# Kernel tuning notes

Measured on AMD Instinct MI355X. Metric: run time of the kernel, lower is better.

## Reference

```python
import jax, jax.numpy as jnp
import numpy as np

N_NODES = 20000
N_EDGES = 640000
D_IN = 128
D_HID = 128


def setup_inputs() -> dict:
    key = jax.random.key(0)
    ks = jax.random.split(key, 10)
    s_in = 1.0 / np.sqrt(D_IN).astype(np.float32)
    s_hid = 1.0 / np.sqrt(D_HID).astype(np.float32)
    return {
        "h": jax.random.normal(ks[0], (N_NODES, D_IN), jnp.float32),
        "edge_index": jax.random.randint(ks[1], (2, N_EDGES), 0, N_NODES, jnp.int32),
        "W0": jax.random.normal(ks[2], (D_IN, D_HID), jnp.float32) * s_in,
        "b0": jnp.zeros((D_HID,), jnp.float32),
        "W1": jax.random.normal(ks[3], (D_HID, D_HID), jnp.float32) * s_hid,
        "b1": jnp.zeros((D_HID,), jnp.float32),
        "W2": jax.random.normal(ks[4], (D_HID, D_HID), jnp.float32) * s_hid,
        "b2": jnp.zeros((D_HID,), jnp.float32),
        "W3": jax.random.normal(ks[5], (D_HID, D_HID), jnp.float32) * s_hid,
        "b3": jnp.zeros((D_HID,), jnp.float32),
    }


def reference(h, edge_index, W0, b0, W1, b1, W2, b2, W3, b3):
    # GIN forward: num_layers-1 = 4 GINConv layers, each
    # h' = Linear((1+eps)*h + sum_{j->i} h_j) with eps = 0.
    src = edge_index[0]
    dst = edge_index[1]
    n = h.shape[0]
    for W, b in ((W0, b0), (W1, b1), (W2, b2), (W3, b3)):
        # sparse sum-aggregation over edges: gather source features, scatter-add to dst
        agg = jax.ops.segment_sum(h[src], dst, num_segments=n)  # [N, D]
        h = (h + agg) @ W + b  # dense per-node MLP (single Linear)
    return h
```

## Files before the change

kernel.cpp:

```cpp
#include <hip/hip_runtime.h>

#define N_NODES 20000
#define N_EDGES 640000
#define D 128
#define CAP 128
#define NB_AGG 40000
#define NB_CHAIN 129
#define SPMV_BLOCKS 313
#define NB_SCAT 625
#define NB_H2BF 1250
#define TM 32

typedef unsigned int uint;
typedef unsigned short ushort;

__device__ __forceinline__ float bflo(uint u) { return __uint_as_float(u << 16); }
__device__ __forceinline__ float bfhi(uint u) { return __uint_as_float(u & 0xffff0000u); }
__device__ __forceinline__ uint pack2bf(float lo, float hi) {
    uint a = __float_as_uint(lo), b = __float_as_uint(hi);
    a += 0x7fffu + ((a >> 16) & 1u);
    b += 0x7fffu + ((b >> 16) & 1u);
    return (a >> 16) | (b & 0xffff0000u);
}


__global__ void zero_cnt_kernel(int* __restrict__ cnt) {
    int i = blockIdx.x * blockDim.x + threadIdx.x;
    if (i < N_NODES) cnt[i] = 0;
}


__global__ void scatter_h2bf_kernel(const int4* __restrict__ src4, const int4* __restrict__ dst4,
                                    int* __restrict__ cnt, ushort* __restrict__ slot,
                                    const float4* __restrict__ hin, uint4* __restrict__ hbf) {
    int bid = blockIdx.x;
    int t = threadIdx.x;
    if (bid < NB_SCAT) {
        int e4 = bid * 256 + t;
        int4 s = src4[e4];
        int4 d = dst4[e4];
        slot[d.x * CAP + atomicAdd(&cnt[d.x], 1)] = (ushort)s.x;
        slot[d.y * CAP + atomicAdd(&cnt[d.y], 1)] = (ushort)s.y;
        slot[d.z * CAP + atomicAdd(&cnt[d.z], 1)] = (ushort)s.z;
        slot[d.w * CAP + atomicAdd(&cnt[d.w], 1)] = (ushort)s.w;
    } else {
        int i = (bid - NB_SCAT) * 256 + t;
        float4 f0 = hin[i * 2];
        float4 f1 = hin[i * 2 + 1];
        uint4 o;
        o.x = pack2bf(f0.x, f0.y); o.y = pack2bf(f0.z, f0.w);
        o.z = pack2bf(f1.x, f1.y); o.w = pack2bf(f1.z, f1.w);
        hbf[i] = o;
    }
}


__global__ __launch_bounds__(64) void agg_fused_kernel(
        const uint4* __restrict__ hbf, const int* __restrict__ cnt,
        const ushort* __restrict__ slot, uint4* __restrict__ xbf,
        const float* __restrict__ cA, const float* __restrict__ cbias,
        const float* __restrict__ cB, float* __restrict__ cO,
        const float* __restrict__ uin, float* __restrict__ uout) {
    int bid = blockIdx.x;
    int t = threadIdx.x;

    if (bid >= NB_AGG) {
        int cb = bid - NB_AGG;
        if (cO && cb < NB_CHAIN) {
            const float* Ar = (cb < 128) ? &cA[cb * 128] : cbias;
            int c0 = t, c1 = t + 64;
            float s0 = 0.f, s1 = 0.f;
            for (int k = 0; k < 128; ++k) {
                float a = Ar[k];
                s0 += a * cB[k * 128 + c0];
                s1 += a * cB[k * 128 + c1];
            }
            cO[cb * 128 + c0] = s0;
            cO[cb * 128 + c1] = s1;
        } else if (uout) {
            int sb = cb - (cO ? NB_CHAIN : 0);
            int node = sb * 64 + t;
            if (node < N_NODES) {
                int c = cnt[node];
                const ushort* sl = &slot[node * CAP];
                float s;
                if (uin) {
                    s = uin[node];
                    for (int k = 0; k < c; ++k) s += uin[sl[k]];
                } else {
                    s = 1.0f + 2.0f * (float)c;
                    for (int k = 0; k < c; ++k) s += (float)cnt[sl[k]];
                }
                uout[node] = s;
            }
        }
        return;
    }

    int r = bid & 7;
    int q = bid >> 3;
    int slice = r >> 2;
    int node  = q * 4 + (r & 3);
    int lo = node * CAP;
    int hi = lo + cnt[node];
    int slot8 = t >> 3;
    int fl    = t & 7;
    int soff  = slice * 8 + fl;

    uint4 sv = hbf[(size_t)node * 16 + soff];

    float a0 = 0.f, a1 = 0.f, a2 = 0.f, a3 = 0.f;
    float a4 = 0.f, a5 = 0.f, a6 = 0.f, a7 = 0.f;

#define ACC8(v) do { \
        a0 += bflo((v).x); a1 += bfhi((v).x); \
        a2 += bflo((v).y); a3 += bfhi((v).y); \
        a4 += bflo((v).z); a5 += bfhi((v).z); \
        a6 += bflo((v).w); a7 += bfhi((v).w); } while (0)

    int k = lo + slot8;
    for (; k + 24 < hi; k += 32) {
        int s0 = slot[k];
        int s1 = slot[k + 8];
        int s2 = slot[k + 16];
        int s3 = slot[k + 24];
        uint4 v0 = hbf[(size_t)s0 * 16 + soff];
        uint4 v1 = hbf[(size_t)s1 * 16 + soff];
        uint4 v2 = hbf[(size_t)s2 * 16 + soff];
        uint4 v3 = hbf[(size_t)s3 * 16 + soff];
        ACC8(v0); ACC8(v1); ACC8(v2); ACC8(v3);
    }
    for (; k < hi; k += 8) {
        int s0 = slot[k];
        uint4 v0 = hbf[(size_t)s0 * 16 + soff];
        ACC8(v0);
    }
#undef ACC8

    a0 += __shfl_xor(a0, 8);  a1 += __shfl_xor(a1, 8);
    a2 += __shfl_xor(a2, 8);  a3 += __shfl_xor(a3, 8);
    a4 += __shfl_xor(a4, 8);  a5 += __shfl_xor(a5, 8);
    a6 += __shfl_xor(a6, 8);  a7 += __shfl_xor(a7, 8);
    a0 += __shfl_xor(a0, 16); a1 += __shfl_xor(a1, 16);
    a2 += __shfl_xor(a2, 16); a3 += __shfl_xor(a3, 16);
    a4 += __shfl_xor(a4, 16); a5 += __shfl_xor(a5, 16);
    a6 += __shfl_xor(a6, 16); a7 += __shfl_xor(a7, 16);
    a0 += __shfl_xor(a0, 32); a1 += __shfl_xor(a1, 32);
    a2 += __shfl_xor(a2, 32); a3 += __shfl_xor(a3, 32);
    a4 += __shfl_xor(a4, 32); a5 += __shfl_xor(a5, 32);
    a6 += __shfl_xor(a6, 32); a7 += __shfl_xor(a7, 32);

    if (t < 8) {
        a0 += bflo(sv.x); a1 += bfhi(sv.x);
        a2 += bflo(sv.y); a3 += bfhi(sv.y);
        a4 += bflo(sv.z); a5 += bfhi(sv.z);
        a6 += bflo(sv.w); a7 += bfhi(sv.w);
        uint4 o;
        o.x = pack2bf(a0, a1); o.y = pack2bf(a2, a3);
        o.z = pack2bf(a4, a5); o.w = pack2bf(a6, a7);
        xbf[(size_t)node * 16 + soff] = o;
    }
}


__global__ __launch_bounds__(256) void gemm_kernel(const uint4* __restrict__ xb,
                                                   const float* __restrict__ W,
                                                   float* __restrict__ out,
                                                   const int* __restrict__ cnt,
                                                   const float* __restrict__ ub,
                                                   const float* __restrict__ uc,
                                                   const float* __restrict__ v2p,
                                                   const float* __restrict__ v3p,
                                                   const float* __restrict__ v4p,
                                                   const float* __restrict__ v1p) {
    __shared__ float Xs[TM][D];
    int t = threadIdx.x;
    int row0 = blockIdx.x * TM;

    for (int i = t; i < TM * 16; i += 256) {
        int rr  = i >> 4;
        int c16 = i & 15;
        uint4 u = xb[(size_t)(row0 + rr) * 16 + c16];
        float4 f0 = make_float4(bflo(u.x), bfhi(u.x), bflo(u.y), bfhi(u.y));
        float4 f1 = make_float4(bflo(u.z), bfhi(u.z), bflo(u.w), bfhi(u.w));
        *((float4*)&Xs[rr][c16 * 8])     = f0;
        *((float4*)&Xs[rr][c16 * 8 + 4]) = f1;
    }
    __syncthreads();

    int cg = t & 31;
    int rg = t >> 5;
    int j0 = cg * 4;
    int r0 = rg * 4;

    float acc[4][4];
    #pragma unroll
    for (int i = 0; i < 4; ++i) {
        acc[i][0] = 0.f; acc[i][1] = 0.f; acc[i][2] = 0.f; acc[i][3] = 0.f;
    }

    for (int k4 = 0; k4 < D; k4 += 4) {
        float4 w0 = *((const float4*)&W[(k4 + 0) * D + j0]);
        float4 w1 = *((const float4*)&W[(k4 + 1) * D + j0]);
        float4 w2 = *((const float4*)&W[(k4 + 2) * D + j0]);
        float4 w3 = *((const float4*)&W[(k4 + 3) * D + j0]);
        #pragma unroll
        for (int i = 0; i < 4; ++i) {
            float4 xv = *((const float4*)&Xs[r0 + i][k4]);
            acc[i][0] += xv.x * w0.x; acc[i][0] += xv.y * w1.x;
            acc[i][0] += xv.z * w2.x; acc[i][0] += xv.w * w3.x;
            acc[i][1] += xv.x * w0.y; acc[i][1] += xv.y * w1.y;
            acc[i][1] += xv.z * w2.y; acc[i][1] += xv.w * w3.y;
            acc[i][2] += xv.x * w0.z; acc[i][2] += xv.y * w1.z;
            acc[i][2] += xv.z * w2.z; acc[i][2] += xv.w * w3.z;
            acc[i][3] += xv.x * w0.w; acc[i][3] += xv.y * w1.w;
            acc[i][3] += xv.z * w2.w; acc[i][3] += xv.w * w3.w;
        }
    }

    float4 v1 = *((const float4*)&v1p[j0]);
    float4 v2 = *((const float4*)&v2p[j0]);
    float4 v3 = *((const float4*)&v3p[j0]);
    float4 v4 = *((const float4*)&v4p[j0]);

    #pragma unroll
    for (int i = 0; i < 4; ++i) {
        int ra = row0 + r0 + i;
        float aa = 1.0f + (float)cnt[ra];
        float ab = ub[ra], ac = uc[ra];
        float o0 = acc[i][0] + ac * v4.x + ab * v3.x + aa * v2.x + v1.x;
        float o1 = acc[i][1] + ac * v4.y + ab * v3.y + aa * v2.y + v1.y;
        float o2 = acc[i][2] + ac * v4.z + ab * v3.z + aa * v2.z + v1.z;
        float o3 = acc[i][3] + ac * v4.w + ab * v3.w + aa * v2.w + v1.w;
        *((float4*)&out[(size_t)ra * D + j0]) = make_float4(o0, o1, o2, o3);
    }
}


extern "C" void kernel_launch(void* const* d_in, const int* in_sizes, int n_in,
                              void* d_out, int out_size, void* d_ws, size_t ws_size,
                              hipStream_t stream) {
    const float* h   = (const float*)d_in[0];
    const int*   ei  = (const int*)d_in[1];
    const int*   src = ei;
    const int*   dst = ei + N_EDGES;
    const float* W0 = (const float*)d_in[2]; const float* b0 = (const float*)d_in[3];
    const float* W1 = (const float*)d_in[4]; const float* b1 = (const float*)d_in[5];
    const float* W2 = (const float*)d_in[6]; const float* b2 = (const float*)d_in[7];
    const float* W3 = (const float*)d_in[8]; const float* b3 = (const float*)d_in[9];
    float* out = (float*)d_out;

    char* ws = (char*)d_ws;
    auto alloc = [&](size_t bytes) {
        char* p = ws;
        ws += (bytes + 255) & ~(size_t)255;
        return p;
    };
    int*    cnt  = (int*)alloc(N_NODES * sizeof(int));
    ushort* slot = (ushort*)alloc((size_t)N_NODES * CAP * sizeof(ushort));
    uint4*  hbf  = (uint4*)alloc((size_t)N_NODES * 16 * sizeof(uint4));
    uint4*  bufA = (uint4*)alloc((size_t)N_NODES * 16 * sizeof(uint4));
    uint4*  bufB = (uint4*)alloc((size_t)N_NODES * 16 * sizeof(uint4));
    float*  T2   = (float*)alloc(129 * D * sizeof(float));
    float*  T3   = (float*)alloc(129 * D * sizeof(float));
    float*  TW   = (float*)alloc(129 * D * sizeof(float));
    float*  ub   = (float*)alloc(N_NODES * sizeof(float));
    float*  uc   = (float*)alloc(N_NODES * sizeof(float));

    zero_cnt_kernel<<<(N_NODES + 255) / 256, 256, 0, stream>>>(cnt);

    scatter_h2bf_kernel<<<NB_SCAT + NB_H2BF, 256, 0, stream>>>(
        (const int4*)src, (const int4*)dst, cnt, slot, (const float4*)h, hbf);

    agg_fused_kernel<<<NB_AGG + NB_CHAIN + SPMV_BLOCKS, 64, 0, stream>>>(
        hbf, cnt, slot, bufA, W2, b2, W3, T2, nullptr, ub);
    agg_fused_kernel<<<NB_AGG + NB_CHAIN + SPMV_BLOCKS, 64, 0, stream>>>(
        bufA, cnt, slot, bufB, W1, b1, T2, T3, ub, uc);
    agg_fused_kernel<<<NB_AGG + NB_CHAIN, 64, 0, stream>>>(
        bufB, cnt, slot, bufA, W0, b0, T3, TW, nullptr, nullptr);
    agg_fused_kernel<<<NB_AGG, 64, 0, stream>>>(
        bufA, cnt, slot, bufB, nullptr, nullptr, nullptr, nullptr, nullptr, nullptr);

    gemm_kernel<<<N_NODES / TM, 256, 0, stream>>>(
        bufB, TW, out, cnt, ub, uc,
        T2 + 128 * D, T3 + 128 * D, TW + 128 * D, b3);
}
```

Measured before the change: 236.0 us.

## Build CSR slots via two-phase bucketed scatter with shared-memory local sort

Replaces direct per-node atomic slot scatter with a two-phase build: edges are first binned into 625 buckets of 32 destination nodes using bucket-level atomics, then a per-bucket kernel distributes them into per-node slots in shared memory and writes the slot array out coalesced. This aims to cut scattered global atomics and random 2-byte global writes, at the cost of an extra kernel launch and an intermediate buffer. Bucket capacity is fixed at 1280 edges, so an unusually skewed destination distribution could overflow it.

```diff
diff --git a/kernel.cpp b/kernel.cpp
--- a/kernel.cpp
+++ b/kernel.cpp
@@ -4,6 +4,8 @@
 #define N_EDGES 640000
 #define D 128
 #define CAP 128
+#define NBK 625
+#define BCAP 1280
 #define NB_AGG 40000
 #define NB_CHAIN 129
 #define SPMV_BLOCKS 313
@@ -24,25 +26,26 @@
 }
 
 
-__global__ void zero_cnt_kernel(int* __restrict__ cnt) {
-    int i = blockIdx.x * blockDim.x + threadIdx.x;
-    if (i < N_NODES) cnt[i] = 0;
-}
-
-
-__global__ void scatter_h2bf_kernel(const int4* __restrict__ src4, const int4* __restrict__ dst4,
-                                    int* __restrict__ cnt, ushort* __restrict__ slot,
-                                    const float4* __restrict__ hin, uint4* __restrict__ hbf) {
+__global__ void zero_bcnt_kernel(int* __restrict__ bcnt) {
+    int i = threadIdx.x;
+    if (i < NBK) bcnt[i] = 0;
+}
+
+
+__global__ void phase1_kernel(const int4* __restrict__ src4, const int4* __restrict__ dst4,
+                              int* __restrict__ bcnt, uint* __restrict__ bbuf,
+                              const float4* __restrict__ hin, uint4* __restrict__ hbf) {
     int bid = blockIdx.x;
     int t = threadIdx.x;
     if (bid < NB_SCAT) {
         int e4 = bid * 256 + t;
         int4 s = src4[e4];
         int4 d = dst4[e4];
-        slot[d.x * CAP + atomicAdd(&cnt[d.x], 1)] = (ushort)s.x;
-        slot[d.y * CAP + atomicAdd(&cnt[d.y], 1)] = (ushort)s.y;
-        slot[d.z * CAP + atomicAdd(&cnt[d.z], 1)] = (ushort)s.z;
-        slot[d.w * CAP + atomicAdd(&cnt[d.w], 1)] = (ushort)s.w;
+        int b;
+        b = d.x >> 5; bbuf[b * BCAP + atomicAdd(&bcnt[b], 1)] = ((uint)(d.x & 31) << 16) | (uint)s.x;
+        b = d.y >> 5; bbuf[b * BCAP + atomicAdd(&bcnt[b], 1)] = ((uint)(d.y & 31) << 16) | (uint)s.y;
+        b = d.z >> 5; bbuf[b * BCAP + atomicAdd(&bcnt[b], 1)] = ((uint)(d.z & 31) << 16) | (uint)s.z;
+        b = d.w >> 5; bbuf[b * BCAP + atomicAdd(&bcnt[b], 1)] = ((uint)(d.w & 31) << 16) | (uint)s.w;
     } else {
         int i = (bid - NB_SCAT) * 256 + t;
         float4 f0 = hin[i * 2];
@@ -52,6 +55,31 @@
         o.z = pack2bf(f1.x, f1.y); o.w = pack2bf(f1.z, f1.w);
         hbf[i] = o;
     }
+}
+
+
+__global__ __launch_bounds__(256) void phase2_kernel(const int* __restrict__ bcnt,
+                                                     const uint* __restrict__ bbuf,
+                                                     int* __restrict__ cnt,
+                                                     ushort* __restrict__ slot) {
+    __shared__ int lcnt[32];
+    __shared__ ushort lslot[32 * CAP];
+    int b = blockIdx.x;
+    int t = threadIdx.x;
+    if (t < 32) lcnt[t] = 0;
+    __syncthreads();
+    int n = bcnt[b];
+    for (int i = t; i < n; i += 256) {
+        uint e = bbuf[b * BCAP + i];
+        int dl = (int)(e >> 16);
+        int p = atomicAdd(&lcnt[dl], 1);
+        lslot[dl * CAP + p] = (ushort)(e & 0xffffu);
+    }
+    __syncthreads();
+    const uint4* ls4 = (const uint4*)lslot;
+    uint4* gs4 = (uint4*)slot + (size_t)b * 32 * CAP / 8;
+    for (int i = t; i < 32 * CAP / 8; i += 256) gs4[i] = ls4[i];
+    if (t < 32) cnt[b * 32 + t] = lcnt[t];
 }
 
 
@@ -257,6 +285,8 @@
         return p;
     };
     int*    cnt  = (int*)alloc(N_NODES * sizeof(int));
+    int*    bcnt = (int*)alloc(NBK * sizeof(int));
+    uint*   bbuf = (uint*)alloc((size_t)NBK * BCAP * sizeof(uint));
     ushort* slot = (ushort*)alloc((size_t)N_NODES * CAP * sizeof(ushort));
     uint4*  hbf  = (uint4*)alloc((size_t)N_NODES * 16 * sizeof(uint4));
     uint4*  bufA = (uint4*)alloc((size_t)N_NODES * 16 * sizeof(uint4));
@@ -267,10 +297,12 @@
     float*  ub   = (float*)alloc(N_NODES * sizeof(float));
     float*  uc   = (float*)alloc(N_NODES * sizeof(float));
 
-    zero_cnt_kernel<<<(N_NODES + 255) / 256, 256, 0, stream>>>(cnt);
-
-    scatter_h2bf_kernel<<<NB_SCAT + NB_H2BF, 256, 0, stream>>>(
-        (const int4*)src, (const int4*)dst, cnt, slot, (const float4*)h, hbf);
+    zero_bcnt_kernel<<<1, 1024, 0, stream>>>(bcnt);
+
+    phase1_kernel<<<NB_SCAT + NB_H2BF, 256, 0, stream>>>(
+        (const int4*)src, (const int4*)dst, bcnt, bbuf, (const float4*)h, hbf);
+
+    phase2_kernel<<<NBK, 256, 0, stream>>>(bcnt, bbuf, cnt, slot);
 
     agg_fused_kernel<<<NB_AGG + NB_CHAIN + SPMV_BLOCKS, 64, 0, stream>>>(
         hbf, cnt, slot, bufA, W2, b2, W3, T2, nullptr, ub);
```

New measurement: 375.0 us. +58.9%, slower.
